# Performance work log

Hardware: AMD Instinct MI355X
Metric: run time of the kernel (lower is better)

## Reference

```python
import jax, jax.numpy as jnp
import numpy as np
from itertools import combinations

MIN_SAMPLES = 200   # min_samples_per_class
MAX_POINTS = 64     # max_points_per_class (cap fed to VR complex)
SCALE = 1.0         # loss_scale_factor
EPS = 1e-12
N_CLASSES = 3


def setup_inputs() -> dict:
    key = jax.random.key(0)
    k1, k2, k3 = jax.random.split(key, 3)
    N, D = 120000, 768
    latent_features = jax.random.normal(k1, (N, D), dtype=jnp.float32)
    labels = jax.random.randint(k2, (N,), 0, N_CLASSES)
    # stand-in for pickled prototype H1 diagrams: [class, points, (birth, death)]
    target_diagrams = jax.random.uniform(k3, (N_CLASSES, 100, 2), dtype=jnp.float32)
    return {"latent_features": latent_features, "labels": labels,
            "target_diagrams": target_diagrams}


def _h1_pairs(Dm):
    """Exact Vietoris-Rips H1 persistence pairing (boundary-matrix reduction).
    Dm: [n,n] numpy distance matrix. Returns (birth_edges [P,2], death_edges [P,2])
    integer index arrays: birth value = Dm[bi,bj] (edge creating the cycle),
    death value = Dm[di,dj] (longest edge of the killing triangle).
    All H1 classes die in the full 2-skeleton, so no essential (inf) points."""
    n = Dm.shape[0]
    ii, jj = np.triu_indices(n, 1)
    vals = Dm[ii, jj]
    order = np.lexsort((jj, ii, vals))        # filtration order of edges
    ei, ej, ev = ii[order], jj[order], vals[order]
    m = ei.shape[0]
    rank = np.zeros((n, n), np.int64)
    rank[ei, ej] = np.arange(m)
    rank[ej, ei] = np.arange(m)
    tris = np.array(list(combinations(range(n), 3)), dtype=np.int64)  # [T,3]
    R = np.stack([rank[tris[:, 0], tris[:, 1]],
                  rank[tris[:, 0], tris[:, 2]],
                  rank[tris[:, 1], tris[:, 2]]], axis=1)              # edge ranks per tri
    maxr = R.max(axis=1)
    tval = ev[maxr]                           # triangle filtration value
    torder = np.lexsort((R[:, 0], R[:, 1], R[:, 2], maxr, tval))
    pivot_col = {}
    births, deaths = [], []
    for t in torder:
        col = set(int(r) for r in R[t])
        while col:
            piv = max(col)                    # low(column) = latest edge
            other = pivot_col.get(piv)
            if other is None:
                pivot_col[piv] = col
                births.append((ei[piv], ej[piv]))
                me = maxr[t]
                deaths.append((ei[me], ej[me]))
                break
            col ^= other                      # Z2 column addition
    if births:
        return np.asarray(births, np.int64), np.asarray(deaths, np.int64)
    return np.zeros((0, 2), np.int64), np.zeros((0, 2), np.int64)


def reference(latent_features, labels, target_diagrams):
    labels_np = np.asarray(labels)
    total = jnp.asarray(0.0, jnp.float32)
    valid = 0
    for c in range(N_CLASSES):
        idx = np.nonzero(labels_np == c)[0]
        if idx.shape[0] < MIN_SAMPLES:
            continue
        idx = idx[:MAX_POINTS]                # deterministic subsample (orig: randperm)
        pts = latent_features[jnp.asarray(idx)]              # [P, D]
        sq = jnp.sum((pts[:, None, :] - pts[None, :, :]) ** 2, axis=-1)
        Dm = jnp.sqrt(jnp.clip(sq, EPS))                     # [P, P] euclidean
        b_idx, d_idx = _h1_pairs(np.asarray(Dm))
        if b_idx.shape[0] > 0:
            tp = jnp.sum(Dm[d_idx[:, 0], d_idx[:, 1]] - Dm[b_idx[:, 0], b_idx[:, 1]])
        else:
            tp = jnp.asarray(0.0, jnp.float32)
        tgt = target_diagrams[c]
        tp_t = jnp.sum(tgt[:, 1] - tgt[:, 0])
        total = total + SCALE * (tp - tp_t) ** 2
        valid += 1
    return total / valid if valid > 0 else jnp.asarray(0.0, jnp.float32)
```

## Files before the change

### kernel.cpp

```cpp
#include <hip/hip_runtime.h>
#include <hip/hip_bf16.h>

#define NCLS 3
#define NPTS 64
#define NEDGE 2016
#define MIN_SAMP 200
#define PENDCAP 128

__device__ int          g_counts[NCLS];
__device__ int          g_sel[NCLS][NPTS];
__device__ float        g_Dm[NCLS][NPTS * NPTS];
__device__ float        g_tp[NCLS];
__device__ int          g_ovf[NCLS];
__device__ unsigned int g_rows[NCLS][NEDGE][64];

__global__ void init_k() {
    if (threadIdx.x < NCLS) { g_counts[threadIdx.x] = 0; g_ovf[threadIdx.x] = 0; }
}

__global__ __launch_bounds__(256) void count_k(const int* __restrict__ labels, int N) {
    __shared__ int c3[NCLS];
    if (threadIdx.x < NCLS) c3[threadIdx.x] = 0;
    __syncthreads();
    for (int i = blockIdx.x * blockDim.x + threadIdx.x; i < N; i += gridDim.x * blockDim.x) {
        int c = labels[i];
        if ((unsigned)c < NCLS) atomicAdd(&c3[c], 1);
    }
    __syncthreads();
    if (threadIdx.x < NCLS) atomicAdd(&g_counts[threadIdx.x], c3[threadIdx.x]);
}

__global__ __launch_bounds__(64) void select_k(const int* __restrict__ labels, int N) {
    const int lane = threadIdx.x;
    int cnt[NCLS] = {0, 0, 0};
    for (int base = 0; base < N; base += 64) {
        if (cnt[0] >= NPTS && cnt[1] >= NPTS && cnt[2] >= NPTS) break;
        int lab = (base + lane < N) ? labels[base + lane] : -1;
        for (int c = 0; c < NCLS; ++c) {
            if (cnt[c] >= NPTS) continue;
            unsigned long long m = __ballot(lab == c);
            if (!m) continue;
            int pos = cnt[c] + __popcll(m & ((1ull << lane) - 1ull));
            if (lab == c && pos < NPTS) g_sel[c][pos] = base + lane;
            cnt[c] = min(NPTS, cnt[c] + (int)__popcll(m));
        }
    }
}

__global__ __launch_bounds__(256) void dist_k(const float* __restrict__ feat) {
    int cls = blockIdx.x;
    if (g_counts[cls] < MIN_SAMP) return;
    int p = blockIdx.y * 256 + threadIdx.x;
    int i = p >> 6, j = p & 63;
    const float4* pi = (const float4*)(feat + (size_t)g_sel[cls][i] * 768);
    const float4* pj = (const float4*)(feat + (size_t)g_sel[cls][j] * 768);
    float sq = 0.f;
    #pragma unroll 4
    for (int d = 0; d < 192; ++d) {
        float4 va = pi[d], vb = pj[d];
        float dx = va.x - vb.x, dy = va.y - vb.y, dz = va.z - vb.z, dw = va.w - vb.w;
        sq = fmaf(dx, dx, sq); sq = fmaf(dy, dy, sq);
        sq = fmaf(dz, dz, sq); sq = fmaf(dw, dw, sq);
    }
    g_Dm[cls][p] = sqrtf(fmaxf(sq, 1e-12f));
}

__device__ __forceinline__ uint4 shfl4(uint4 v, int src) {
    uint4 r;
    r.x = (unsigned)__shfl((int)v.x, src);
    r.y = (unsigned)__shfl((int)v.y, src);
    r.z = (unsigned)__shfl((int)v.z, src);
    r.w = (unsigned)__shfl((int)v.w, src);
    return r;
}
__device__ __forceinline__ void xor4(uint4& a, const uint4 b) {
    a.x ^= b.x; a.y ^= b.y; a.z ^= b.z; a.w ^= b.w;
}
__device__ __forceinline__ unsigned int getw4(const uint4 a, int m) {
    return (m < 32) ? a.x : (m < 64) ? a.y : (m < 96) ? a.z : a.w;
}
__device__ __forceinline__ void set4(uint4& a, int m) {
    const unsigned int b = 1u << (m & 31);
    if (m < 32) a.x |= b; else if (m < 64) a.y |= b; else if (m < 96) a.z |= b; else a.w |= b;
}

__device__ __forceinline__ uint4 pend_apply(uint4 v, const uint4 pm,
                                            const uint4* s_pend, const unsigned char* s_pidx) {
    unsigned int w;
    w = v.x & pm.x;
    while (w) { int c = __builtin_ctz(w); w &= w - 1; xor4(v, s_pend[s_pidx[c]]); }
    w = v.y & pm.y;
    while (w) { int c = __builtin_ctz(w); w &= w - 1; xor4(v, s_pend[s_pidx[32 + c]]); }
    w = v.z & pm.z;
    while (w) { int c = __builtin_ctz(w); w &= w - 1; xor4(v, s_pend[s_pidx[64 + c]]); }
    w = v.w & pm.w;
    while (w) { int c = __builtin_ctz(w); w &= w - 1; xor4(v, s_pend[s_pidx[96 + c]]); }
    return v;
}

__global__ __launch_bounds__(1024) void persist_fast_k() {
    const int cls  = blockIdx.x;
    const int tid  = threadIdx.x;
    const int lane = tid & 63;
    const int wid  = tid >> 6;
    if (g_counts[cls] < MIN_SAMP) return;

    __shared__ union UA {
        float sDm[NPTS * NPTS];
        uint4 M[NEDGE];
    } uA;
    __shared__ short         rank2d[NPTS * NPTS];
    __shared__ unsigned char se_i[NEDGE], se_j[NEDGE];
    __shared__ float         ev[NEDGE];
    __shared__ unsigned char e2i[NEDGE], e2j[NEDGE];
    __shared__ uint4         s_pend[PENDCAP];
    __shared__ unsigned char s_pidx[128];

    for (int p = tid; p < NPTS * NPTS; p += 1024) uA.sDm[p] = g_Dm[cls][p];
    if (tid < NPTS - 1) {
        int i = tid;
        int base = i * (2 * NPTS - 1 - i) / 2;
        for (int j = i + 1; j < NPTS; ++j) {
            e2i[base + j - i - 1] = (unsigned char)i;
            e2j[base + j - i - 1] = (unsigned char)j;
        }
    }
    if (tid < NPTS) rank2d[tid * NPTS + tid] = 0x7fff;
    __syncthreads();

    for (int e = tid; e < NEDGE; e += 1024) {
        int i_ = e2i[e], j_ = e2j[e];
        float v = uA.sDm[i_ * NPTS + j_];
        int rk = 0;
        for (int f = 0; f < NEDGE; ++f) {
            int fi = e2i[f], fj = e2j[f];
            float w = uA.sDm[fi * NPTS + fj];
            bool less = (w < v) || (w == v && (fi < i_ || (fi == i_ && fj < j_)));
            rk += less ? 1 : 0;
        }
        se_i[rk] = (unsigned char)i_;
        se_j[rk] = (unsigned char)j_;
        ev[rk]   = v;
        rank2d[i_ * NPTS + j_] = (short)rk;
        rank2d[j_ * NPTS + i_] = (short)rk;
    }
    __syncthreads();

    if (wid != 0) return;

    int   rootv = lane;
    uint4 occ      = make_uint4(0u, 0u, 0u, 0u);
    uint4 pendmask = make_uint4(0u, 0u, 0u, 0u);
    int   pcount = 0, inuse = 0, bail = 0;
    double birth = 0.0, death = 0.0;

    for (int r = 0; r < NEDGE; ++r) {
        if (pcount >= 64 || inuse >= 126) {
            for (int x = lane; x < r; x += 64) {
                uint4 row = uA.M[x];
                const unsigned int anyw = (row.x & pendmask.x) | (row.y & pendmask.y)
                                        | (row.z & pendmask.z) | (row.w & pendmask.w);
                if (anyw) uA.M[x] = pend_apply(row, pendmask, s_pend, s_pidx);
            }
            occ.x &= ~pendmask.x; occ.y &= ~pendmask.y;
            occ.z &= ~pendmask.z; occ.w &= ~pendmask.w;
            inuse -= pcount; pcount = 0;
            pendmask = make_uint4(0u, 0u, 0u, 0u);
            if (inuse >= 127) { bail = 1; break; }
        }

        const int i_ = se_i[r], j_ = se_j[r];
        const float evr = ev[r];

        const int rootI = __shfl(rootv, i_);
        const int rootJ = __shfl(rootv, j_);
        uint4 ann = make_uint4(0u, 0u, 0u, 0u);
        if (rootI != rootJ) {
            rootv = (rootv == rootI) ? rootJ : rootv;
        } else {
            birth += (double)evr;
            int s = (~occ.x) ? __builtin_ctz(~occ.x)
                  : (~occ.y) ? 32 + __builtin_ctz(~occ.y)
                  : (~occ.z) ? 64 + __builtin_ctz(~occ.z)
                  : (~occ.w) ? 96 + __builtin_ctz(~occ.w) : -1;
            if (s < 0) { bail = 1; break; }
            set4(occ, s); ++inuse;
            set4(ann, s);
        }
        if (lane == 0) uA.M[r] = ann;

        const int a_l = rank2d[i_ * NPTS + lane];
        const int b_l = rank2d[j_ * NPTS + lane];
        const bool validk = (lane != i_) && (lane != j_) && (a_l < r) && (b_l < r);
        if (!__ballot(validk)) continue;

        uint4 v = make_uint4(0u, 0u, 0u, 0u);
        if (validk) {
            v = uA.M[a_l];
            xor4(v, uA.M[b_l]);
            xor4(v, ann);
            v = pend_apply(v, pendmask, s_pend, s_pidx);
        }

        uint4 s4 = make_uint4(0u, 0u, 0u, 0u);
        int accidx = -1, accm = 0;
        int d = 0;
        while (true) {
            unsigned long long nzm = __ballot((v.x | v.y | v.z | v.w) != 0u);
            if (!nzm) break;
            const int l = __builtin_ctzll(nzm);
            const uint4 p = shfl4(v, l);
            const int m = p.x ? __builtin_ctz(p.x) : p.y ? 32 + __builtin_ctz(p.y)
                       : p.z ? 64 + __builtin_ctz(p.z) : 96 + __builtin_ctz(p.w);
            if (lane == l) { s4 = v; accidx = d; accm = m; }
            const unsigned int mb2 = 1u << (m & 31);
            if (getw4(v, m) & mb2) xor4(v, p);
            if (accidx >= 0 && accidx < d) {
                if (getw4(s4, m) & mb2) xor4(s4, p);
            }
            ++d;
        }
        if (d == 0) continue;
        death += (double)d * (double)evr;

        const int pbase = pcount;
        if (accidx >= 0) {
            s_pend[pbase + accidx] = s4;
            s_pidx[accm] = (unsigned char)(pbase + accidx);
        }
        for (int t = 0; t < d; ++t) {
            const unsigned long long who = __ballot(accidx == t);
            const int l = __builtin_ctzll(who);
            const int m = __shfl(accm, l);
            const uint4 u4 = shfl4(s4, l);
            set4(pendmask, m);
            const unsigned int mb2 = 1u << (m & 31);
            for (int x = lane; x < pbase; x += 64) {
                uint4 q = s_pend[x];
                if (getw4(q, m) & mb2) { xor4(q, u4); s_pend[x] = q; }
            }
        }
        pcount += d;
    }

    if (lane == 0) {
        if (bail) g_ovf[cls] = 1;
        else      g_tp[cls] = (float)(death - birth);
    }
}

__global__ __launch_bounds__(1024) void persist_exact_k() {
    const int cls  = blockIdx.x;
    const int tid  = threadIdx.x;
    const int lane = tid & 63;
    const int wid  = tid >> 6;
    if (g_counts[cls] < MIN_SAMP) return;
    if (!g_ovf[cls]) return;

    union PhaseU {
        float        sDm[NPTS * NPTS];
        unsigned int pbuf[62][64];
    };
    __shared__ PhaseU        u;
    __shared__ short         rank2d[NPTS * NPTS];
    __shared__ unsigned char e2i[NEDGE], e2j[NEDGE];
    __shared__ unsigned char se_i[NEDGE], se_j[NEDGE];
    __shared__ float         ev[NEDGE];
    __shared__ unsigned char cstate[64];
    __shared__ int           s_t;
    __shared__ double        s_birth, s_death;
    __shared__ unsigned char parent[NPTS];

    for (int p = tid; p < NPTS * NPTS; p += 1024) u.sDm[p] = g_Dm[cls][p];
    if (tid < NPTS - 1) {
        int i = tid;
        int base = i * (2 * NPTS - 1 - i) / 2;
        for (int j = i + 1; j < NPTS; ++j) {
            e2i[base + j - i - 1] = (unsigned char)i;
            e2j[base + j - i - 1] = (unsigned char)j;
        }
    }
    for (int x = tid; x < NEDGE * 64; x += 1024) {
        int rr = x >> 6, w = x & 63;
        g_rows[cls][rr][w] = (w == (rr >> 5)) ? (1u << (rr & 31)) : 0u;
    }
    if (tid < NPTS) rank2d[tid * NPTS + tid] = 0x7fff;
    __syncthreads();

    for (int e = tid; e < NEDGE; e += 1024) {
        int i_ = e2i[e], j_ = e2j[e];
        float v = u.sDm[i_ * NPTS + j_];
        int rk = 0;
        for (int f = 0; f < NEDGE; ++f) {
            int fi = e2i[f], fj = e2j[f];
            float w = u.sDm[fi * NPTS + fj];
            bool less = (w < v) || (w == v && (fi < i_ || (fi == i_ && fj < j_)));
            rk += less ? 1 : 0;
        }
        se_i[rk] = (unsigned char)i_;
        se_j[rk] = (unsigned char)j_;
        ev[rk]   = v;
        rank2d[i_ * NPTS + j_] = (short)rk;
        rank2d[j_ * NPTS + i_] = (short)rk;
    }
    __syncthreads();

    if (tid == 0) {
        for (int i = 0; i < NPTS; ++i) parent[i] = (unsigned char)i;
        double bs = 0.0;
        for (int r = 0; r < NEDGE; ++r) {
            int x = se_i[r]; while (parent[x] != x) { parent[x] = parent[parent[x]]; x = parent[x]; }
            int y = se_j[r]; while (parent[y] != y) { parent[y] = parent[parent[y]]; y = parent[y]; }
            if (x == y) bs += (double)ev[r];
            else parent[x] = (unsigned char)y;
        }
        s_birth = bs; s_death = 0.0;
    }
    __syncthreads();

    unsigned int (*Row)[64] = g_rows[cls];

    for (int r = 1; r < NEDGE; ++r) {
        const int i_ = se_i[r], j_ = se_j[r];
        const int a_l = rank2d[i_ * NPTS + lane];
        const int b_l = rank2d[j_ * NPTS + lane];
        const bool valid = (lane != i_) && (lane != j_) && (a_l < r) && (b_l < r);
        const unsigned long long mask = __ballot(valid);
        if (!mask) continue;
        const int cnt = __popcll(mask);

        {
            const unsigned int rrow = Row[r][lane];
            for (int idx = wid; idx < cnt; idx += 16) {
                unsigned long long mm = mask;
                for (int s = 0; s < idx; ++s) mm &= mm - 1;
                const int k = __builtin_ctzll(mm);
                const int a = __shfl(a_l, k);
                const int b = __shfl(b_l, k);
                const unsigned int p = Row[a][lane] ^ Row[b][lane] ^ rrow;
                u.pbuf[idx][lane] = p;
                const bool indep = (__ballot(p != 0u) != 0ull);
                if (lane == 0) cstate[idx] = indep ? 1 : 0;
            }
        }
        __syncthreads();

        while (true) {
            int c = -1;
            for (int x = 0; x < cnt; ++x) if (cstate[x] == 1) { c = x; break; }
            if (c < 0) break;
            __syncthreads();
            if (wid == 0) {
                const unsigned int pw = u.pbuf[c][lane];
                const unsigned long long m2 = __ballot(pw != 0u);
                const int fl = __builtin_ctzll(m2);
                const unsigned int w0 = (unsigned int)__shfl((int)pw, fl);
                if (lane == 0) s_t = fl * 32 + __builtin_ctz(w0);
            }
            if (tid == 0) { s_death += (double)ev[r]; cstate[c] = 2; }
            __syncthreads();
            const int t = s_t, tw = t >> 5;
            const unsigned int tb = 1u << (t & 31);
            const unsigned int pw = u.pbuf[c][lane];
            for (int rr0 = wid * 64; rr0 < NEDGE; rr0 += 1024) {
                const int rr = rr0 + lane;
                unsigned int hit = (rr < NEDGE) ? (Row[rr][tw] & tb) : 0u;
                unsigned long long mrows = __ballot(hit != 0u);
                while (mrows) {
                    const int rx = rr0 + __builtin_ctzll(mrows);
                    mrows &= mrows - 1;
                    Row[rx][lane] ^= pw;
                }
            }
            __threadfence_block();
            __syncthreads();
            {
                const unsigned int rrow2 = Row[r][lane];
                for (int idx = wid; idx < cnt; idx += 16) {
                    if (cstate[idx] != 1) continue;
                    unsigned long long mm = mask;
                    for (int s = 0; s < idx; ++s) mm &= mm - 1;
                    const int k = __builtin_ctzll(mm);
                    const int a = __shfl(a_l, k);
                    const int b = __shfl(b_l, k);
                    const unsigned int p2 = Row[a][lane] ^ Row[b][lane] ^ rrow2;
                    u.pbuf[idx][lane] = p2;
                    const bool indep = (__ballot(p2 != 0u) != 0ull);
                    if (lane == 0) cstate[idx] = indep ? 1 : 0;
                }
            }
            __syncthreads();
        }
        __syncthreads();
    }

    if (tid == 0) g_tp[cls] = (float)(s_death - s_birth);
}

__global__ void final_k(const float* __restrict__ tgt, float* __restrict__ out) {
    double total = 0.0;
    int valid = 0;
    for (int c = 0; c < NCLS; ++c) {
        if (g_counts[c] >= MIN_SAMP) {
            double tpt = 0.0;
            for (int p = 0; p < 100; ++p)
                tpt += (double)tgt[(c * 100 + p) * 2 + 1] - (double)tgt[(c * 100 + p) * 2 + 0];
            double d = (double)g_tp[c] - tpt;
            total += d * d;
            valid++;
        }
    }
    *out = valid ? (float)(total / valid) : 0.0f;
}

extern "C" void kernel_launch(void* const* d_in, const int* in_sizes, int n_in,
                              void* d_out, int out_size, void* d_ws, size_t ws_size,
                              hipStream_t stream) {
    const float* feat   = (const float*)d_in[0];
    const int*   labels = (const int*)d_in[1];
    const float* tgt    = (const float*)d_in[2];
    const int N = in_sizes[1];

    hipLaunchKernelGGL(init_k,         dim3(1),        dim3(64),   0, stream);
    hipLaunchKernelGGL(count_k,        dim3(256),      dim3(256),  0, stream, labels, N);
    hipLaunchKernelGGL(select_k,       dim3(1),        dim3(64),   0, stream, labels, N);
    hipLaunchKernelGGL(dist_k,         dim3(NCLS, 16), dim3(256),  0, stream, feat);
    hipLaunchKernelGGL(persist_fast_k, dim3(NCLS),     dim3(1024), 0, stream);
    hipLaunchKernelGGL(persist_exact_k,dim3(NCLS),     dim3(1024), 0, stream);
    hipLaunchKernelGGL(final_k,        dim3(1),        dim3(1),    0, stream, tgt, (float*)d_out);
}
```

Before: 2.843 ms.

## Batch edges in blocks of 16 and build triangle candidates across all warps

The single-warp sequential edge sweep becomes a blocked scheme. All 16 warps redundantly track union-find state for each group of 16 edges, and each warp builds the candidate triangle columns for one edge. The candidates are compacted into shared memory and then reduced by warp 0. This spreads the column-gathering and pending-apply work across the whole block, at the cost of several block-wide barriers per 16 edges, more shared memory, and a lower flush threshold that may trigger the exact fallback path more often.

Measured after the change: 2.377 ms (median of 2 runs). 1.2x faster.

```diff
diff --git a/kernel.cpp b/kernel.cpp
--- a/kernel.cpp
+++ b/kernel.cpp
@@ -6,6 +6,8 @@
 #define NEDGE 2016
 #define MIN_SAMP 200
 #define PENDCAP 128
+#define BLK 16
+#define MAXCAND (BLK * 62)
 
 __device__ int          g_counts[NCLS];
 __device__ int          g_sel[NCLS][NPTS];
@@ -115,6 +117,11 @@
     __shared__ unsigned char e2i[NEDGE], e2j[NEDGE];
     __shared__ uint4         s_pend[PENDCAP];
     __shared__ unsigned char s_pidx[128];
+    __shared__ uint4         vbuf[MAXCAND];
+    __shared__ unsigned char gidb[MAXCAND];
+    __shared__ int           s_cnt[BLK];
+    __shared__ uint4         s_npm;
+    __shared__ int           s_d, s_ovf;
 
     for (int p = tid; p < NPTS * NPTS; p += 1024) uA.sDm[p] = g_Dm[cls][p];
     if (tid < NPTS - 1) {
@@ -146,17 +153,15 @@
     }
     __syncthreads();
 
-    if (wid != 0) return;
-
-    int   rootv = lane;
-    uint4 occ      = make_uint4(0u, 0u, 0u, 0u);
-    uint4 pendmask = make_uint4(0u, 0u, 0u, 0u);
-    int   pcount = 0, inuse = 0, bail = 0;
+    int    rootv = lane;
+    uint4  occ      = make_uint4(0u, 0u, 0u, 0u);
+    uint4  pendmask = make_uint4(0u, 0u, 0u, 0u);
+    int    pcount = 0, inuse = 0, bail = 0;
     double birth = 0.0, death = 0.0;
 
-    for (int r = 0; r < NEDGE; ++r) {
-        if (pcount >= 64 || inuse >= 126) {
-            for (int x = lane; x < r; x += 64) {
+    for (int r = 0; r < NEDGE; r += BLK) {
+        if (pcount >= 48 || inuse >= 110) {
+            for (int x = tid; x < r; x += 1024) {
                 uint4 row = uA.M[x];
                 const unsigned int anyw = (row.x & pendmask.x) | (row.y & pendmask.y)
                                         | (row.z & pendmask.z) | (row.w & pendmask.w);
@@ -166,84 +171,131 @@
             occ.z &= ~pendmask.z; occ.w &= ~pendmask.w;
             inuse -= pcount; pcount = 0;
             pendmask = make_uint4(0u, 0u, 0u, 0u);
-            if (inuse >= 127) { bail = 1; break; }
-        }
-
-        const int i_ = se_i[r], j_ = se_j[r];
-        const float evr = ev[r];
-
-        const int rootI = __shfl(rootv, i_);
-        const int rootJ = __shfl(rootv, j_);
-        uint4 ann = make_uint4(0u, 0u, 0u, 0u);
-        if (rootI != rootJ) {
-            rootv = (rootv == rootI) ? rootJ : rootv;
-        } else {
-            birth += (double)evr;
-            int s = (~occ.x) ? __builtin_ctz(~occ.x)
-                  : (~occ.y) ? 32 + __builtin_ctz(~occ.y)
-                  : (~occ.z) ? 64 + __builtin_ctz(~occ.z)
-                  : (~occ.w) ? 96 + __builtin_ctz(~occ.w) : -1;
-            if (s < 0) { bail = 1; break; }
-            set4(occ, s); ++inuse;
-            set4(ann, s);
-        }
-        if (lane == 0) uA.M[r] = ann;
-
-        const int a_l = rank2d[i_ * NPTS + lane];
-        const int b_l = rank2d[j_ * NPTS + lane];
-        const bool validk = (lane != i_) && (lane != j_) && (a_l < r) && (b_l < r);
-        if (!__ballot(validk)) continue;
+            __syncthreads();
+            if (inuse >= 110) { bail = 1; break; }
+        }
+
+        for (int t = 0; t < BLK; ++t) {
+            const int g = r + t;
+            const int i_ = se_i[g], j_ = se_j[g];
+            const int rootI = __shfl(rootv, i_);
+            const int rootJ = __shfl(rootv, j_);
+            uint4 ann = make_uint4(0u, 0u, 0u, 0u);
+            if (rootI != rootJ) {
+                rootv = (rootv == rootI) ? rootJ : rootv;
+            } else {
+                birth += (double)ev[g];
+                int s = (~occ.x) ? __builtin_ctz(~occ.x)
+                      : (~occ.y) ? 32 + __builtin_ctz(~occ.y)
+                      : (~occ.z) ? 64 + __builtin_ctz(~occ.z)
+                      : (~occ.w) ? 96 + __builtin_ctz(~occ.w) : -1;
+                if (s < 0) { bail = 1; }
+                else { set4(occ, s); ++inuse; set4(ann, s); }
+            }
+            if (tid == t) uA.M[g] = ann;
+        }
+        if (bail) break;
+        __syncthreads();
 
         uint4 v = make_uint4(0u, 0u, 0u, 0u);
-        if (validk) {
-            v = uA.M[a_l];
-            xor4(v, uA.M[b_l]);
-            xor4(v, ann);
-            v = pend_apply(v, pendmask, s_pend, s_pidx);
-        }
-
-        uint4 s4 = make_uint4(0u, 0u, 0u, 0u);
-        int accidx = -1, accm = 0;
-        int d = 0;
-        while (true) {
-            unsigned long long nzm = __ballot((v.x | v.y | v.z | v.w) != 0u);
-            if (!nzm) break;
-            const int l = __builtin_ctzll(nzm);
-            const uint4 p = shfl4(v, l);
-            const int m = p.x ? __builtin_ctz(p.x) : p.y ? 32 + __builtin_ctz(p.y)
-                       : p.z ? 64 + __builtin_ctz(p.z) : 96 + __builtin_ctz(p.w);
-            if (lane == l) { s4 = v; accidx = d; accm = m; }
-            const unsigned int mb2 = 1u << (m & 31);
-            if (getw4(v, m) & mb2) xor4(v, p);
-            if (accidx >= 0 && accidx < d) {
-                if (getw4(s4, m) & mb2) xor4(s4, p);
-            }
-            ++d;
-        }
-        if (d == 0) continue;
-        death += (double)d * (double)evr;
-
-        const int pbase = pcount;
-        if (accidx >= 0) {
-            s_pend[pbase + accidx] = s4;
-            s_pidx[accm] = (unsigned char)(pbase + accidx);
-        }
-        for (int t = 0; t < d; ++t) {
-            const unsigned long long who = __ballot(accidx == t);
-            const int l = __builtin_ctzll(who);
-            const int m = __shfl(accm, l);
-            const uint4 u4 = shfl4(s4, l);
-            set4(pendmask, m);
-            const unsigned int mb2 = 1u << (m & 31);
-            for (int x = lane; x < pbase; x += 64) {
-                uint4 q = s_pend[x];
-                if (getw4(q, m) & mb2) { xor4(q, u4); s_pend[x] = q; }
-            }
-        }
-        pcount += d;
-    }
-
-    if (lane == 0) {
+        unsigned long long mask;
+        {
+            const int g = r + wid;
+            const int i_ = se_i[g], j_ = se_j[g];
+            const short a_l = rank2d[i_ * NPTS + lane];
+            const short b_l = rank2d[j_ * NPTS + lane];
+            const bool valid = (lane != i_) && (lane != j_) && (a_l < g) && (b_l < g);
+            mask = __ballot(valid);
+            if (lane == 0) s_cnt[wid] = (int)__popcll(mask);
+            if (valid) {
+                v = uA.M[a_l];
+                xor4(v, uA.M[b_l]);
+                { uint4 t4 = uA.M[g]; xor4(v, t4); }
+                v = pend_apply(v, pendmask, s_pend, s_pidx);
+            }
+        }
+        __syncthreads();
+
+        int base = 0, tot = 0;
+        #pragma unroll
+        for (int t2 = 0; t2 < BLK; ++t2) {
+            const int c = s_cnt[t2];
+            if (t2 < wid) base += c;
+            tot += c;
+        }
+        if ((mask >> lane) & 1ull) {
+            const int pos = base + (int)__popcll(mask & ((1ull << lane) - 1ull));
+            vbuf[pos] = v;
+            gidb[pos] = (unsigned char)wid;
+        }
+        __syncthreads();
+
+        if (wid == 0) {
+            uint4 npmB = make_uint4(0u, 0u, 0u, 0u);
+            int dB = 0, ovf = 0;
+            for (int c0 = 0; c0 < tot; c0 += 64) {
+                const int n = (tot - c0 < 64) ? (tot - c0) : 64;
+                uint4 v2 = make_uint4(0u, 0u, 0u, 0u);
+                float evl = 0.f;
+                if (lane < n) {
+                    v2 = vbuf[c0 + lane];
+                    evl = ev[r + gidb[c0 + lane]];
+                    v2 = pend_apply(v2, npmB, s_pend, s_pidx);
+                }
+                uint4 s4 = make_uint4(0u, 0u, 0u, 0u);
+                int accidx = -1, accm = 0, d = 0;
+                while (true) {
+                    unsigned long long nzm = __ballot((v2.x | v2.y | v2.z | v2.w) != 0u);
+                    if (!nzm) break;
+                    const int l = __builtin_ctzll(nzm);
+                    const uint4 p = shfl4(v2, l);
+                    const float evp = __shfl(evl, l);
+                    const int m = p.x ? __builtin_ctz(p.x) : p.y ? 32 + __builtin_ctz(p.y)
+                               : p.z ? 64 + __builtin_ctz(p.z) : 96 + __builtin_ctz(p.w);
+                    if (lane == l) { s4 = v2; accidx = d; accm = m; }
+                    const unsigned int mb2 = 1u << (m & 31);
+                    if (getw4(v2, m) & mb2) xor4(v2, p);
+                    if (accidx >= 0 && accidx < d) {
+                        if (getw4(s4, m) & mb2) xor4(s4, p);
+                    }
+                    death += (double)evp;
+                    ++d;
+                }
+                if (d) {
+                    const int pbase = pcount + dB;
+                    if (pbase + d > PENDCAP) { ovf = 1; break; }
+                    if (accidx >= 0) {
+                        s_pend[pbase + accidx] = s4;
+                        s_pidx[accm] = (unsigned char)(pbase + accidx);
+                    }
+                    for (int t3 = 0; t3 < d; ++t3) {
+                        const unsigned long long who = __ballot(accidx == t3);
+                        const int l = __builtin_ctzll(who);
+                        const int m = __shfl(accm, l);
+                        const uint4 u4 = shfl4(s4, l);
+                        set4(npmB, m);
+                        const unsigned int mb2 = 1u << (m & 31);
+                        for (int x = lane; x < pbase; x += 64) {
+                            uint4 q = s_pend[x];
+                            if (getw4(q, m) & mb2) { xor4(q, u4); s_pend[x] = q; }
+                        }
+                    }
+                    dB += d;
+                }
+            }
+            if (lane == 0) { s_npm = npmB; s_d = dB; s_ovf = ovf; }
+        }
+        __syncthreads();
+        {
+            const uint4 npm = s_npm;
+            pendmask.x |= npm.x; pendmask.y |= npm.y;
+            pendmask.z |= npm.z; pendmask.w |= npm.w;
+            pcount += s_d;
+            if (s_ovf) { bail = 1; break; }
+        }
+    }
+
+    if (wid == 0 && lane == 0) {
         if (bail) g_ovf[cls] = 1;
         else      g_tp[cls] = (float)(death - birth);
     }
```
